# Optimization experiments

Hardware: AMD Instinct MI355X
Metric: run time of the kernel (lower is better)

## Reference

```python
import jax, jax.numpy as jnp
import numpy as np

N, D, O, E = 100000, 32, 64, 1600000

def setup_inputs() -> dict:
    key = jax.random.key(0)
    ks = jax.random.split(key, 6)
    x = jax.random.normal(ks[0], (N, D), dtype=jnp.float32)
    edge_index = jax.random.randint(ks[1], (2, E), 0, N, dtype=jnp.int64)
    edge_attr = jax.random.uniform(ks[2], (E, 1), dtype=jnp.float32)
    # nodec MLP params (stored as [in, out]; equiv to torch Linear weight.T)
    W1 = jax.random.normal(ks[3], (3 * D, O), dtype=jnp.float32) * (1.0 / np.sqrt(3 * D))
    b1 = jnp.zeros((O,), dtype=jnp.float32)
    W2 = jax.random.normal(ks[4], (O, O), dtype=jnp.float32) * (1.0 / np.sqrt(O))
    b2 = jnp.zeros((O,), dtype=jnp.float32)
    return {"x": x, "edge_index": edge_index, "edge_attr": edge_attr,
            "W1": W1, "b1": b1, "W2": W2, "b2": b2}

def reference(x, edge_index, edge_attr, W1, b1, W2, b2):
    row, col = edge_index[0], edge_index[1]
    n = x.shape[0]
    # gather, weight by edge_attr, scatter-add into destination nodes
    mi = jax.ops.segment_sum(edge_attr * x[row], col, num_segments=n)  # [N, D]
    mo = jax.ops.segment_sum(edge_attr * x[col], row, num_segments=n)  # [N, D]
    M = jnp.concatenate([mi, mo, x], axis=-1)  # [N, 3D]
    h = jnp.tanh(M @ W1 + b1)
    return jnp.tanh(h @ W2 + b2)
```

## Files before the change

### kernel.cpp

```cpp
#include <hip/hip_runtime.h>
#include <hip/hip_bf16.h>


#define DFEAT 32
#define OFEAT 64
#define EPB   2048
#define KEYS_PER_BIN 128
#define MAXBIN 2048
#define CAP   3072

typedef unsigned long long u64;

__device__ __forceinline__ float rdlane(float v, int l) {
    return __int_as_float(__builtin_amdgcn_readlane(__float_as_int(v), l));
}

__global__ __launch_bounds__(256) void hist_part(
    const int* __restrict__ ei, int* __restrict__ blockhist, int E, int NBIN)
{
    __shared__ int lh[MAXBIN];
    int blk = blockIdx.x;
    for (int i = threadIdx.x; i < NBIN; i += 256) lh[i] = 0;
    __syncthreads();
    int e0 = blk * EPB;
    #pragma unroll
    for (int j = 0; j < 8; ++j) {
        int e = e0 + j * 256 + threadIdx.x;
        if (e < E) {
            int r = ei[e], c = ei[E + e];
            atomicAdd(&lh[(2 * c) >> 7], 1);
            atomicAdd(&lh[(2 * r + 1) >> 7], 1);
        }
    }
    __syncthreads();
    for (int i = threadIdx.x; i < NBIN; i += 256)
        blockhist[(long long)blk * NBIN + i] = lh[i];
}

__global__ __launch_bounds__(64) void colscan(
    const int* __restrict__ blockhist, int* __restrict__ ofsT,
    int* __restrict__ bintotal, int nPB, int NBIN)
{
    int bin  = blockIdx.x;
    int lane = threadIdx.x;
    int run = 0;
    for (int b0 = 0; b0 < nPB; b0 += 64) {
        int b = b0 + lane;
        int v = (b < nPB) ? blockhist[(long long)b * NBIN + bin] : 0;
        int s = v;
        #pragma unroll
        for (int d = 1; d < 64; d <<= 1) {
            int t = __shfl_up(s, d, 64);
            if (lane >= d) s += t;
        }
        if (b < nPB) ofsT[(long long)bin * nPB + b] = s - v + run;
        run += __shfl(s, 63, 64);
    }
    if (lane == 0) bintotal[bin] = run;
}

__global__ __launch_bounds__(1024) void scan_bins(
    const int* __restrict__ bintotal, int* __restrict__ binbase, int NBIN)
{
    __shared__ int s[1024];
    int t = threadIdx.x;
    int i0 = 2 * t, i1 = 2 * t + 1;
    int p0 = (i0 < NBIN) ? ((bintotal[i0] + 1) & ~1) : 0;
    int p1 = (i1 < NBIN) ? ((bintotal[i1] + 1) & ~1) : 0;
    int v = p0 + p1;
    s[t] = v;
    __syncthreads();
    for (int o = 1; o < 1024; o <<= 1) {
        int u = (t >= o) ? s[t - o] : 0;
        __syncthreads();
        s[t] += u;
        __syncthreads();
    }
    int excl = s[t] - v;
    if (i0 < NBIN) binbase[i0] = excl;
    if (i1 < NBIN) binbase[i1] = excl + p0;
}

__global__ __launch_bounds__(256) void partition_kernel(
    const int* __restrict__ ei, const float* __restrict__ ea,
    const int* __restrict__ ofsT, const int* __restrict__ binbase,
    u64* __restrict__ pay, int E, int NBIN, int nPB)
{
    __shared__ int lofs[MAXBIN + 1];
    __shared__ int lcur[MAXBIN];
    __shared__ int lbase[MAXBIN];
    __shared__ u64 stag[2 * EPB];
    __shared__ unsigned short binof[2 * EPB];
    int blk = blockIdx.x, tid = threadIdx.x;
    int e0 = blk * EPB;

    for (int i = tid; i < NBIN; i += 256) lcur[i] = 0;
    __syncthreads();

    int r[8], c[8]; float a[8]; bool valid[8];
    #pragma unroll
    for (int j = 0; j < 8; ++j) {
        int e = e0 + j * 256 + tid;
        valid[j] = (e < E);
        if (valid[j]) {
            r[j] = ei[e]; c[j] = ei[E + e]; a[j] = ea[e];
            atomicAdd(&lcur[(2 * c[j]) >> 7], 1);
            atomicAdd(&lcur[(2 * r[j] + 1) >> 7], 1);
        }
    }
    __syncthreads();

    if (tid < 64) {
        int runc = 0;
        for (int b0 = 0; b0 < NBIN; b0 += 64) {
            int i = b0 + tid;
            int v = (i < NBIN) ? lcur[i] : 0;
            int s = v;
            #pragma unroll
            for (int d = 1; d < 64; d <<= 1) {
                int t2 = __shfl_up(s, d, 64);
                if (tid >= d) s += t2;
            }
            if (i < NBIN) lofs[i] = s - v + runc;
            runc += __shfl(s, 63, 64);
        }
        if (tid == 0) lofs[NBIN] = runc;
    }
    __syncthreads();

    for (int i = tid; i < NBIN; i += 256) {
        lcur[i] = 0;
        lbase[i] = binbase[i] + ofsT[(long long)i * nPB + blk];
    }
    __syncthreads();

    #pragma unroll
    for (int j = 0; j < 8; ++j) {
        if (valid[j]) {
            unsigned int ab = (unsigned int)__float_as_int(a[j]);
            {
                int key = 2 * c[j]; int bin = key >> 7;
                int t2 = atomicAdd(&lcur[bin], 1);
                int pos = lofs[bin] + t2;
                stag[pos] = ((u64)ab << 32) |
                    (unsigned int)(r[j] | ((key & 127) << 17));
                binof[pos] = (unsigned short)bin;
            }
            {
                int key = 2 * r[j] + 1; int bin = key >> 7;
                int t2 = atomicAdd(&lcur[bin], 1);
                int pos = lofs[bin] + t2;
                stag[pos] = ((u64)ab << 32) |
                    (unsigned int)(c[j] | ((key & 127) << 17));
                binof[pos] = (unsigned short)bin;
            }
        }
    }
    __syncthreads();

    int total = lofs[NBIN];
    for (int i = tid; i < total; i += 256) {
        int bn = binof[i];
        pay[lbase[bn] + (i - lofs[bn])] = stag[i];
    }
}

__global__ __launch_bounds__(512) void accum_sortgather(
    const float* __restrict__ x,
    const int* __restrict__ binbase, const int* __restrict__ bintotal,
    const u64* __restrict__ pay,
    float* __restrict__ mi, float* __restrict__ mo, int NK)
{
    __shared__ u64 srec[CAP];
    __shared__ int lcnt[KEYS_PER_BIN];
    __shared__ int lofs[KEYS_PER_BIN];
    __shared__ int lcur[KEYS_PER_BIN];

    int b = blockIdx.x, tid = threadIdx.x;
    int base = binbase[b];
    int n    = bintotal[b];
    int wid  = tid >> 6;
    int lane = tid & 63;
    int half = lane >> 5;
    int feat = lane & 31;

    float accA[4], accB[4], accC[4], accD[4];
    #pragma unroll
    for (int p = 0; p < 4; ++p) {
        accA[p] = 0.0f; accB[p] = 0.0f; accC[p] = 0.0f; accD[p] = 0.0f;
    }

    for (int c0 = 0; c0 < n; c0 += CAP) {
        int cn = min(n - c0, CAP);
        if (tid < KEYS_PER_BIN) lcnt[tid] = 0;
        __syncthreads();
        for (int i = tid; i < cn; i += 512)
            atomicAdd(&lcnt[((int)pay[base + c0 + i] >> 17) & 127], 1);
        __syncthreads();
        if (tid < 64) {
            int v0 = lcnt[2 * tid], v1 = lcnt[2 * tid + 1];
            int s = v0 + v1, ss = s;
            #pragma unroll
            for (int d = 1; d < 64; d <<= 1) {
                int t = __shfl_up(ss, d, 64);
                if (tid >= d) ss += t;
            }
            int excl = ss - s;
            lofs[2 * tid] = excl;      lofs[2 * tid + 1] = excl + v0;
            lcur[2 * tid] = excl;      lcur[2 * tid + 1] = excl + v0;
        }
        __syncthreads();
        for (int i = tid; i < cn; i += 512) {
            u64 v = pay[base + c0 + i];
            int t2 = atomicAdd(&lcur[((int)v >> 17) & 127], 1);
            srec[t2] = v;
        }
        __syncthreads();

        #pragma unroll
        for (int p = 0; p < 4; ++p) {
            int kb = wid * 16 + 4 * p;
            int s0 = lofs[kb + 0], e0 = s0 + lcnt[kb + 0];
            int s1 = lofs[kb + 1], e1 = s1 + lcnt[kb + 1];
            int s2 = lofs[kb + 2], e2 = s2 + lcnt[kb + 2];
            int s3 = lofs[kb + 3], e3 = s3 + lcnt[kb + 3];
            int i0 = s0 + half, i1 = s1 + half, i2 = s2 + half, i3 = s3 + half;
            float a0 = accA[p], a1 = accB[p], a2 = accC[p], a3 = accD[p];
            while (i0 < e0 && i1 < e1 && i2 < e2 && i3 < e3) {
                u64 r0 = srec[i0], r1 = srec[i1], r2 = srec[i2], r3 = srec[i3];
                float x0 = x[(long long)((int)r0 & 0x1FFFF) * DFEAT + feat];
                float x1 = x[(long long)((int)r1 & 0x1FFFF) * DFEAT + feat];
                float x2 = x[(long long)((int)r2 & 0x1FFFF) * DFEAT + feat];
                float x3 = x[(long long)((int)r3 & 0x1FFFF) * DFEAT + feat];
                a0 = fmaf(__int_as_float((int)(r0 >> 32)), x0, a0);
                a1 = fmaf(__int_as_float((int)(r1 >> 32)), x1, a1);
                a2 = fmaf(__int_as_float((int)(r2 >> 32)), x2, a2);
                a3 = fmaf(__int_as_float((int)(r3 >> 32)), x3, a3);
                i0 += 2; i1 += 2; i2 += 2; i3 += 2;
            }
            while (i0 < e0) {
                u64 rr = srec[i0];
                a0 = fmaf(__int_as_float((int)(rr >> 32)),
                          x[(long long)((int)rr & 0x1FFFF) * DFEAT + feat], a0);
                i0 += 2;
            }
            while (i1 < e1) {
                u64 rr = srec[i1];
                a1 = fmaf(__int_as_float((int)(rr >> 32)),
                          x[(long long)((int)rr & 0x1FFFF) * DFEAT + feat], a1);
                i1 += 2;
            }
            while (i2 < e2) {
                u64 rr = srec[i2];
                a2 = fmaf(__int_as_float((int)(rr >> 32)),
                          x[(long long)((int)rr & 0x1FFFF) * DFEAT + feat], a2);
                i2 += 2;
            }
            while (i3 < e3) {
                u64 rr = srec[i3];
                a3 = fmaf(__int_as_float((int)(rr >> 32)),
                          x[(long long)((int)rr & 0x1FFFF) * DFEAT + feat], a3);
                i3 += 2;
            }
            accA[p] = a0; accB[p] = a1; accC[p] = a2; accD[p] = a3;
        }
        __syncthreads();
    }

    int key0 = b * KEYS_PER_BIN + wid * 16;
    #pragma unroll
    for (int p = 0; p < 4; ++p) {
        float t0 = accA[p] + __shfl_xor(accA[p], 32, 64);
        float t1 = accB[p] + __shfl_xor(accB[p], 32, 64);
        float t2 = accC[p] + __shfl_xor(accC[p], 32, 64);
        float t3 = accD[p] + __shfl_xor(accD[p], 32, 64);
        float vA = half ? t2 : t0;
        float vB = half ? t3 : t1;
        int gkA = key0 + 4 * p + (half ? 2 : 0);
        int gkB = gkA + 1;
        if (gkA < NK) {
            int node = gkA >> 1;
            ((gkA & 1) ? mo : mi)[(long long)node * DFEAT + feat] = vA;
        }
        if (gkB < NK) {
            int node = gkB >> 1;
            ((gkB & 1) ? mo : mi)[(long long)node * DFEAT + feat] = vB;
        }
    }
}

__global__ __launch_bounds__(256) void edge_scatter_kernel(
    const float* __restrict__ x, const int* __restrict__ ei,
    const float* __restrict__ ea,
    float* __restrict__ mi, float* __restrict__ mo, int E)
{
    long long tid = (long long)blockIdx.x * blockDim.x + threadIdx.x;
    long long total = (long long)E * 8;
    if (tid >= total) return;
    int e = (int)(tid >> 3);
    int q = (int)(tid & 7);
    int r = ei[e];
    int c = ei[E + e];
    float a = ea[e];
    const float4* x4 = (const float4*)x;
    float4 xr = x4[(long long)r * 8 + q];
    float4 xc = x4[(long long)c * 8 + q];
    float* mip = mi + (long long)c * DFEAT + q * 4;
    float* mop = mo + (long long)r * DFEAT + q * 4;
    atomicAdd(mip + 0, a * xr.x); atomicAdd(mip + 1, a * xr.y);
    atomicAdd(mip + 2, a * xr.z); atomicAdd(mip + 3, a * xr.w);
    atomicAdd(mop + 0, a * xc.x); atomicAdd(mop + 1, a * xc.y);
    atomicAdd(mop + 2, a * xc.z); atomicAdd(mop + 3, a * xc.w);
}

__global__ __launch_bounds__(256) void mlp_reg_kernel(
    const float* __restrict__ mi, const float* __restrict__ mo,
    const float* __restrict__ x,
    const float* __restrict__ W1, const float* __restrict__ b1,
    const float* __restrict__ W2, const float* __restrict__ b2,
    float* __restrict__ out, int N)
{
    int o   = threadIdx.x & 63;
    int wid = threadIdx.x >> 6;

    float w1r[96], w2r[64];
    #pragma unroll
    for (int k = 0; k < 96; ++k) w1r[k] = W1[k * 64 + o];
    #pragma unroll
    for (int k = 0; k < 64; ++k) w2r[k] = W2[k * 64 + o];
    float bias1 = b1[o];
    float bias2 = b2[o];

    int stride = gridDim.x * 4;
    for (int node = blockIdx.x * 4 + wid; node < N; node += stride) {
        long long nb = (long long)node * DFEAT;
        float m01 = (o < 32) ? mi[nb + o] : mo[nb + (o - 32)];
        float m2v = (o < 32) ? x[nb + o] : 0.0f;

        float a0 = bias1, a1 = 0.0f, a2 = 0.0f, a3 = 0.0f;
        #pragma unroll
        for (int k = 0; k < 64; k += 4) {
            a0 = fmaf(rdlane(m01, k + 0), w1r[k + 0], a0);
            a1 = fmaf(rdlane(m01, k + 1), w1r[k + 1], a1);
            a2 = fmaf(rdlane(m01, k + 2), w1r[k + 2], a2);
            a3 = fmaf(rdlane(m01, k + 3), w1r[k + 3], a3);
        }
        #pragma unroll
        for (int k = 0; k < 32; k += 4) {
            a0 = fmaf(rdlane(m2v, k + 0), w1r[64 + k + 0], a0);
            a1 = fmaf(rdlane(m2v, k + 1), w1r[64 + k + 1], a1);
            a2 = fmaf(rdlane(m2v, k + 2), w1r[64 + k + 2], a2);
            a3 = fmaf(rdlane(m2v, k + 3), w1r[64 + k + 3], a3);
        }
        float h = tanhf(((a0 + a1) + (a2 + a3)));

        float c0 = bias2, c1 = 0.0f, c2 = 0.0f, c3 = 0.0f;
        #pragma unroll
        for (int k = 0; k < 64; k += 4) {
            c0 = fmaf(rdlane(h, k + 0), w2r[k + 0], c0);
            c1 = fmaf(rdlane(h, k + 1), w2r[k + 1], c1);
            c2 = fmaf(rdlane(h, k + 2), w2r[k + 2], c2);
            c3 = fmaf(rdlane(h, k + 3), w2r[k + 3], c3);
        }
        out[(long long)node * OFEAT + o] = tanhf(((c0 + c1) + (c2 + c3)));
    }
}

extern "C" void kernel_launch(void* const* d_in, const int* in_sizes, int n_in,
                              void* d_out, int out_size, void* d_ws, size_t ws_size,
                              hipStream_t stream) {
    const float* x  = (const float*)d_in[0];
    const int*   ei = (const int*)  d_in[1];
    const float* ea = (const float*)d_in[2];
    const float* W1 = (const float*)d_in[3];
    const float* b1 = (const float*)d_in[4];
    const float* W2 = (const float*)d_in[5];
    const float* b2 = (const float*)d_in[6];
    float* out = (float*)d_out;

    int N    = in_sizes[0] / DFEAT;
    int E    = in_sizes[2];
    int NK   = 2 * N;
    int NBIN = (NK + KEYS_PER_BIN - 1) / KEYS_PER_BIN;
    int nPB  = (E + EPB - 1) / EPB;

    float* mi = (float*)d_ws;
    float* mo = mi + (size_t)N * DFEAT;

    size_t paySlots = (size_t)2 * E + NBIN;
    size_t need = (size_t)N * DFEAT * 2 * 4
                + paySlots * 8
                + (size_t)nPB * NBIN * 4 * 2
                + (size_t)NBIN * 4 * 2 + 64;

    if (ws_size >= need && N <= (1 << 17) && NBIN <= MAXBIN) {
        u64* pay       = (u64*)(mo + (size_t)N * DFEAT);
        int* blockhist = (int*)(pay + paySlots);
        int* ofsT      = blockhist + (size_t)nPB * NBIN;
        int* bintotal  = ofsT + (size_t)nPB * NBIN;
        int* binbase   = bintotal + NBIN;

        hist_part<<<nPB, 256, 0, stream>>>(ei, blockhist, E, NBIN);
        colscan<<<NBIN, 64, 0, stream>>>(blockhist, ofsT, bintotal, nPB, NBIN);
        scan_bins<<<1, 1024, 0, stream>>>(bintotal, binbase, NBIN);
        partition_kernel<<<nPB, 256, 0, stream>>>(ei, ea, ofsT, binbase,
                                                  pay, E, NBIN, nPB);
        accum_sortgather<<<NBIN, 512, 0, stream>>>(x, binbase, bintotal, pay,
                                                   mi, mo, NK);
    } else {
        hipMemsetAsync(d_ws, 0, (size_t)N * DFEAT * 2 * sizeof(float), stream);
        long long total = (long long)E * 8;
        int nblocks = (int)((total + 255) / 256);
        edge_scatter_kernel<<<nblocks, 256, 0, stream>>>(x, ei, ea, mi, mo, E);
    }

    mlp_reg_kernel<<<512, 256, 0, stream>>>(mi, mo, x, W1, b1, W2, b2, out, N);
}
```

Baseline: 236.1 us.

## Vectorize edge loads, shrink partition LDS, and grid-stride bin accumulation

The histogram and partition kernels now run 512 threads per block, each loading four consecutive edges with int4/float4 vector loads. Partition drops the per-record bin-id array and stores offsets as 16-bit values, finding each record's bin by binary search over the offsets. This cuts LDS use, which may raise occupancy, at the cost of extra search work in the scatter loop. The accumulation kernel launches half as many blocks and loops over bins grid-stride, so two bins run back to back per block.

New measurement: 262.9 us. 11.4% more time.

```diff
diff --git a/kernel.cpp b/kernel.cpp
--- a/kernel.cpp
+++ b/kernel.cpp
@@ -6,7 +6,7 @@
 #define OFEAT 64
 #define EPB   2048
 #define KEYS_PER_BIN 128
-#define MAXBIN 2048
+#define NBINMAX 1568
 #define CAP   3072
 
 typedef unsigned long long u64;
@@ -15,25 +15,33 @@
     return __int_as_float(__builtin_amdgcn_readlane(__float_as_int(v), l));
 }
 
-__global__ __launch_bounds__(256) void hist_part(
+__global__ __launch_bounds__(512) void hist_part(
     const int* __restrict__ ei, int* __restrict__ blockhist, int E, int NBIN)
 {
-    __shared__ int lh[MAXBIN];
-    int blk = blockIdx.x;
-    for (int i = threadIdx.x; i < NBIN; i += 256) lh[i] = 0;
+    __shared__ int lh[NBINMAX];
+    int blk = blockIdx.x, tid = threadIdx.x;
+    for (int i = tid; i < NBIN; i += 512) lh[i] = 0;
     __syncthreads();
     int e0 = blk * EPB;
-    #pragma unroll
-    for (int j = 0; j < 8; ++j) {
-        int e = e0 + j * 256 + threadIdx.x;
-        if (e < E) {
-            int r = ei[e], c = ei[E + e];
-            atomicAdd(&lh[(2 * c) >> 7], 1);
-            atomicAdd(&lh[(2 * r + 1) >> 7], 1);
-        }
-    }
-    __syncthreads();
-    for (int i = threadIdx.x; i < NBIN; i += 256)
+    if (e0 + EPB <= E) {
+        int4 rr = *(const int4*)(ei + e0 + tid * 4);
+        int4 cc = *(const int4*)(ei + E + e0 + tid * 4);
+        atomicAdd(&lh[(2 * cc.x) >> 7], 1); atomicAdd(&lh[(2 * rr.x + 1) >> 7], 1);
+        atomicAdd(&lh[(2 * cc.y) >> 7], 1); atomicAdd(&lh[(2 * rr.y + 1) >> 7], 1);
+        atomicAdd(&lh[(2 * cc.z) >> 7], 1); atomicAdd(&lh[(2 * rr.z + 1) >> 7], 1);
+        atomicAdd(&lh[(2 * cc.w) >> 7], 1); atomicAdd(&lh[(2 * rr.w + 1) >> 7], 1);
+    } else {
+        #pragma unroll
+        for (int j = 0; j < 4; ++j) {
+            int e = e0 + tid * 4 + j;
+            if (e < E) {
+                atomicAdd(&lh[(2 * ei[E + e]) >> 7], 1);
+                atomicAdd(&lh[(2 * ei[e] + 1) >> 7], 1);
+            }
+        }
+    }
+    __syncthreads();
+    for (int i = tid; i < NBIN; i += 512)
         blockhist[(long long)blk * NBIN + i] = lh[i];
 }
 
@@ -81,32 +89,44 @@
     if (i1 < NBIN) binbase[i1] = excl + p0;
 }
 
-__global__ __launch_bounds__(256) void partition_kernel(
+__global__ __launch_bounds__(512) void partition_kernel(
     const int* __restrict__ ei, const float* __restrict__ ea,
     const int* __restrict__ ofsT, const int* __restrict__ binbase,
     u64* __restrict__ pay, int E, int NBIN, int nPB)
 {
-    __shared__ int lofs[MAXBIN + 1];
-    __shared__ int lcur[MAXBIN];
-    __shared__ int lbase[MAXBIN];
+    __shared__ unsigned short lofsw[NBINMAX + 1];
+    __shared__ int lcur[NBINMAX];
+    __shared__ int lbase[NBINMAX];
     __shared__ u64 stag[2 * EPB];
-    __shared__ unsigned short binof[2 * EPB];
     int blk = blockIdx.x, tid = threadIdx.x;
     int e0 = blk * EPB;
 
-    for (int i = tid; i < NBIN; i += 256) lcur[i] = 0;
-    __syncthreads();
-
-    int r[8], c[8]; float a[8]; bool valid[8];
-    #pragma unroll
-    for (int j = 0; j < 8; ++j) {
-        int e = e0 + j * 256 + tid;
-        valid[j] = (e < E);
-        if (valid[j]) {
-            r[j] = ei[e]; c[j] = ei[E + e]; a[j] = ea[e];
-            atomicAdd(&lcur[(2 * c[j]) >> 7], 1);
-            atomicAdd(&lcur[(2 * r[j] + 1) >> 7], 1);
-        }
+    for (int i = tid; i < NBIN; i += 512) lcur[i] = 0;
+    __syncthreads();
+
+    int4 rr, cc; float4 av; bool full = (e0 + EPB <= E);
+    if (full) {
+        rr = *(const int4*)(ei + e0 + tid * 4);
+        cc = *(const int4*)(ei + E + e0 + tid * 4);
+        av = *(const float4*)(ea + e0 + tid * 4);
+        atomicAdd(&lcur[(2 * cc.x) >> 7], 1); atomicAdd(&lcur[(2 * rr.x + 1) >> 7], 1);
+        atomicAdd(&lcur[(2 * cc.y) >> 7], 1); atomicAdd(&lcur[(2 * rr.y + 1) >> 7], 1);
+        atomicAdd(&lcur[(2 * cc.z) >> 7], 1); atomicAdd(&lcur[(2 * rr.z + 1) >> 7], 1);
+        atomicAdd(&lcur[(2 * cc.w) >> 7], 1); atomicAdd(&lcur[(2 * rr.w + 1) >> 7], 1);
+    } else {
+        int rs[4], cs[4]; float as[4];
+        #pragma unroll
+        for (int j = 0; j < 4; ++j) {
+            int e = e0 + tid * 4 + j;
+            if (e < E) {
+                rs[j] = ei[e]; cs[j] = ei[E + e]; as[j] = ea[e];
+                atomicAdd(&lcur[(2 * cs[j]) >> 7], 1);
+                atomicAdd(&lcur[(2 * rs[j] + 1) >> 7], 1);
+            } else { rs[j] = 0; cs[j] = 0; as[j] = 0.0f; }
+        }
+        rr = make_int4(rs[0], rs[1], rs[2], rs[3]);
+        cc = make_int4(cs[0], cs[1], cs[2], cs[3]);
+        av = make_float4(as[0], as[1], as[2], as[3]);
     }
     __syncthreads();
 
@@ -121,47 +141,53 @@
                 int t2 = __shfl_up(s, d, 64);
                 if (tid >= d) s += t2;
             }
-            if (i < NBIN) lofs[i] = s - v + runc;
+            if (i < NBIN) lofsw[i] = (unsigned short)(s - v + runc);
             runc += __shfl(s, 63, 64);
         }
-        if (tid == 0) lofs[NBIN] = runc;
-    }
-    __syncthreads();
-
-    for (int i = tid; i < NBIN; i += 256) {
+        if (tid == 0) lofsw[NBIN] = (unsigned short)runc;
+    }
+    __syncthreads();
+
+    for (int i = tid; i < NBIN; i += 512) {
         lcur[i] = 0;
         lbase[i] = binbase[i] + ofsT[(long long)i * nPB + blk];
     }
     __syncthreads();
 
-    #pragma unroll
-    for (int j = 0; j < 8; ++j) {
-        if (valid[j]) {
-            unsigned int ab = (unsigned int)__float_as_int(a[j]);
-            {
-                int key = 2 * c[j]; int bin = key >> 7;
-                int t2 = atomicAdd(&lcur[bin], 1);
-                int pos = lofs[bin] + t2;
-                stag[pos] = ((u64)ab << 32) |
-                    (unsigned int)(r[j] | ((key & 127) << 17));
-                binof[pos] = (unsigned short)bin;
-            }
-            {
-                int key = 2 * r[j] + 1; int bin = key >> 7;
-                int t2 = atomicAdd(&lcur[bin], 1);
-                int pos = lofs[bin] + t2;
-                stag[pos] = ((u64)ab << 32) |
-                    (unsigned int)(c[j] | ((key & 127) << 17));
-                binof[pos] = (unsigned short)bin;
-            }
-        }
-    }
-    __syncthreads();
-
-    int total = lofs[NBIN];
-    for (int i = tid; i < total; i += 256) {
-        int bn = binof[i];
-        pay[lbase[bn] + (i - lofs[bn])] = stag[i];
+    {
+        int rs[4] = {rr.x, rr.y, rr.z, rr.w};
+        int cs[4] = {cc.x, cc.y, cc.z, cc.w};
+        float as[4] = {av.x, av.y, av.z, av.w};
+        #pragma unroll
+        for (int j = 0; j < 4; ++j) {
+            int e = e0 + tid * 4 + j;
+            if (e < E) {
+                unsigned int ab = (unsigned int)__float_as_int(as[j]);
+                {
+                    int key = 2 * cs[j]; int bin = key >> 7;
+                    int t2 = atomicAdd(&lcur[bin], 1);
+                    stag[(int)lofsw[bin] + t2] = ((u64)ab << 32) |
+                        (unsigned int)(rs[j] | ((key & 127) << 17));
+                }
+                {
+                    int key = 2 * rs[j] + 1; int bin = key >> 7;
+                    int t2 = atomicAdd(&lcur[bin], 1);
+                    stag[(int)lofsw[bin] + t2] = ((u64)ab << 32) |
+                        (unsigned int)(cs[j] | ((key & 127) << 17));
+                }
+            }
+        }
+    }
+    __syncthreads();
+
+    int total = lofsw[NBIN];
+    for (int i = tid; i < total; i += 512) {
+        int lo = 0, hi = NBIN;
+        while (hi - lo > 1) {
+            int mid = (lo + hi) >> 1;
+            if ((int)lofsw[mid] <= i) lo = mid; else hi = mid;
+        }
+        pay[lbase[lo] + (i - (int)lofsw[lo])] = stag[i];
     }
 }
 
@@ -169,123 +195,127 @@
     const float* __restrict__ x,
     const int* __restrict__ binbase, const int* __restrict__ bintotal,
     const u64* __restrict__ pay,
-    float* __restrict__ mi, float* __restrict__ mo, int NK)
+    float* __restrict__ mi, float* __restrict__ mo, int NK, int NBIN)
 {
     __shared__ u64 srec[CAP];
     __shared__ int lcnt[KEYS_PER_BIN];
     __shared__ int lofs[KEYS_PER_BIN];
     __shared__ int lcur[KEYS_PER_BIN];
 
-    int b = blockIdx.x, tid = threadIdx.x;
-    int base = binbase[b];
-    int n    = bintotal[b];
+    int tid = threadIdx.x;
     int wid  = tid >> 6;
     int lane = tid & 63;
     int half = lane >> 5;
     int feat = lane & 31;
 
-    float accA[4], accB[4], accC[4], accD[4];
-    #pragma unroll
-    for (int p = 0; p < 4; ++p) {
-        accA[p] = 0.0f; accB[p] = 0.0f; accC[p] = 0.0f; accD[p] = 0.0f;
-    }
-
-    for (int c0 = 0; c0 < n; c0 += CAP) {
-        int cn = min(n - c0, CAP);
-        if (tid < KEYS_PER_BIN) lcnt[tid] = 0;
+    for (int b = blockIdx.x; b < NBIN; b += gridDim.x) {
+        int base = binbase[b];
+        int n    = bintotal[b];
+
+        float accA[4], accB[4], accC[4], accD[4];
+        #pragma unroll
+        for (int p = 0; p < 4; ++p) {
+            accA[p] = 0.0f; accB[p] = 0.0f; accC[p] = 0.0f; accD[p] = 0.0f;
+        }
+
+        for (int c0 = 0; c0 < n; c0 += CAP) {
+            int cn = min(n - c0, CAP);
+            if (tid < KEYS_PER_BIN) lcnt[tid] = 0;
+            __syncthreads();
+            for (int i = tid; i < cn; i += 512)
+                atomicAdd(&lcnt[((int)pay[base + c0 + i] >> 17) & 127], 1);
+            __syncthreads();
+            if (tid < 64) {
+                int v0 = lcnt[2 * tid], v1 = lcnt[2 * tid + 1];
+                int s = v0 + v1, ss = s;
+                #pragma unroll
+                for (int d = 1; d < 64; d <<= 1) {
+                    int t = __shfl_up(ss, d, 64);
+                    if (tid >= d) ss += t;
+                }
+                int excl = ss - s;
+                lofs[2 * tid] = excl;      lofs[2 * tid + 1] = excl + v0;
+                lcur[2 * tid] = excl;      lcur[2 * tid + 1] = excl + v0;
+            }
+            __syncthreads();
+            for (int i = tid; i < cn; i += 512) {
+                u64 v = pay[base + c0 + i];
+                int t2 = atomicAdd(&lcur[((int)v >> 17) & 127], 1);
+                srec[t2] = v;
+            }
+            __syncthreads();
+
+            #pragma unroll
+            for (int p = 0; p < 4; ++p) {
+                int kb = wid * 16 + 4 * p;
+                int s0 = lofs[kb + 0], e0 = s0 + lcnt[kb + 0];
+                int s1 = lofs[kb + 1], e1 = s1 + lcnt[kb + 1];
+                int s2 = lofs[kb + 2], e2 = s2 + lcnt[kb + 2];
+                int s3 = lofs[kb + 3], e3 = s3 + lcnt[kb + 3];
+                int i0 = s0 + half, i1 = s1 + half, i2 = s2 + half, i3 = s3 + half;
+                float a0 = accA[p], a1 = accB[p], a2 = accC[p], a3 = accD[p];
+                while (i0 < e0 && i1 < e1 && i2 < e2 && i3 < e3) {
+                    u64 r0 = srec[i0], r1 = srec[i1], r2 = srec[i2], r3 = srec[i3];
+                    float x0 = x[(long long)((int)r0 & 0x1FFFF) * DFEAT + feat];
+                    float x1 = x[(long long)((int)r1 & 0x1FFFF) * DFEAT + feat];
+                    float x2 = x[(long long)((int)r2 & 0x1FFFF) * DFEAT + feat];
+                    float x3 = x[(long long)((int)r3 & 0x1FFFF) * DFEAT + feat];
+                    a0 = fmaf(__int_as_float((int)(r0 >> 32)), x0, a0);
+                    a1 = fmaf(__int_as_float((int)(r1 >> 32)), x1, a1);
+                    a2 = fmaf(__int_as_float((int)(r2 >> 32)), x2, a2);
+                    a3 = fmaf(__int_as_float((int)(r3 >> 32)), x3, a3);
+                    i0 += 2; i1 += 2; i2 += 2; i3 += 2;
+                }
+                while (i0 < e0) {
+                    u64 rr = srec[i0];
+                    a0 = fmaf(__int_as_float((int)(rr >> 32)),
+                              x[(long long)((int)rr & 0x1FFFF) * DFEAT + feat], a0);
+                    i0 += 2;
+                }
+                while (i1 < e1) {
+                    u64 rr = srec[i1];
+                    a1 = fmaf(__int_as_float((int)(rr >> 32)),
+                              x[(long long)((int)rr & 0x1FFFF) * DFEAT + feat], a1);
+                    i1 += 2;
+                }
+                while (i2 < e2) {
+                    u64 rr = srec[i2];
+                    a2 = fmaf(__int_as_float((int)(rr >> 32)),
+                              x[(long long)((int)rr & 0x1FFFF) * DFEAT + feat], a2);
+                    i2 += 2;
+                }
+                while (i3 < e3) {
+                    u64 rr = srec[i3];
+                    a3 = fmaf(__int_as_float((int)(rr >> 32)),
+                              x[(long long)((int)rr & 0x1FFFF) * DFEAT + feat], a3);
+                    i3 += 2;
+                }
+                accA[p] = a0; accB[p] = a1; accC[p] = a2; accD[p] = a3;
+            }
+            __syncthreads();
+        }
+
+        int key0 = b * KEYS_PER_BIN + wid * 16;
+        #pragma unroll
+        for (int p = 0; p < 4; ++p) {
+            float t0 = accA[p] + __shfl_xor(accA[p], 32, 64);
+            float t1 = accB[p] + __shfl_xor(accB[p], 32, 64);
+            float t2 = accC[p] + __shfl_xor(accC[p], 32, 64);
+            float t3 = accD[p] + __shfl_xor(accD[p], 32, 64);
+            float vA = half ? t2 : t0;
+            float vB = half ? t3 : t1;
+            int gkA = key0 + 4 * p + (half ? 2 : 0);
+            int gkB = gkA + 1;
+            if (gkA < NK) {
+                int node = gkA >> 1;
+                ((gkA & 1) ? mo : mi)[(long long)node * DFEAT + feat] = vA;
+            }
+            if (gkB < NK) {
+                int node = gkB >> 1;
+                ((gkB & 1) ? mo : mi)[(long long)node * DFEAT + feat] = vB;
+            }
+        }
         __syncthreads();
-        for (int i = tid; i < cn; i += 512)
-            atomicAdd(&lcnt[((int)pay[base + c0 + i] >> 17) & 127], 1);
-        __syncthreads();
-        if (tid < 64) {
-            int v0 = lcnt[2 * tid], v1 = lcnt[2 * tid + 1];
-            int s = v0 + v1, ss = s;
-            #pragma unroll
-            for (int d = 1; d < 64; d <<= 1) {
-                int t = __shfl_up(ss, d, 64);
-                if (tid >= d) ss += t;
-            }
-            int excl = ss - s;
-            lofs[2 * tid] = excl;      lofs[2 * tid + 1] = excl + v0;
-            lcur[2 * tid] = excl;      lcur[2 * tid + 1] = excl + v0;
-        }
-        __syncthreads();
-        for (int i = tid; i < cn; i += 512) {
-            u64 v = pay[base + c0 + i];
-            int t2 = atomicAdd(&lcur[((int)v >> 17) & 127], 1);
-            srec[t2] = v;
-        }
-        __syncthreads();
-
-        #pragma unroll
-        for (int p = 0; p < 4; ++p) {
-            int kb = wid * 16 + 4 * p;
-            int s0 = lofs[kb + 0], e0 = s0 + lcnt[kb + 0];
-            int s1 = lofs[kb + 1], e1 = s1 + lcnt[kb + 1];
-            int s2 = lofs[kb + 2], e2 = s2 + lcnt[kb + 2];
-            int s3 = lofs[kb + 3], e3 = s3 + lcnt[kb + 3];
-            int i0 = s0 + half, i1 = s1 + half, i2 = s2 + half, i3 = s3 + half;
-            float a0 = accA[p], a1 = accB[p], a2 = accC[p], a3 = accD[p];
-            while (i0 < e0 && i1 < e1 && i2 < e2 && i3 < e3) {
-                u64 r0 = srec[i0], r1 = srec[i1], r2 = srec[i2], r3 = srec[i3];
-                float x0 = x[(long long)((int)r0 & 0x1FFFF) * DFEAT + feat];
-                float x1 = x[(long long)((int)r1 & 0x1FFFF) * DFEAT + feat];
-                float x2 = x[(long long)((int)r2 & 0x1FFFF) * DFEAT + feat];
-                float x3 = x[(long long)((int)r3 & 0x1FFFF) * DFEAT + feat];
-                a0 = fmaf(__int_as_float((int)(r0 >> 32)), x0, a0);
-                a1 = fmaf(__int_as_float((int)(r1 >> 32)), x1, a1);
-                a2 = fmaf(__int_as_float((int)(r2 >> 32)), x2, a2);
-                a3 = fmaf(__int_as_float((int)(r3 >> 32)), x3, a3);
-                i0 += 2; i1 += 2; i2 += 2; i3 += 2;
-            }
-            while (i0 < e0) {
-                u64 rr = srec[i0];
-                a0 = fmaf(__int_as_float((int)(rr >> 32)),
-                          x[(long long)((int)rr & 0x1FFFF) * DFEAT + feat], a0);
-                i0 += 2;
-            }
-            while (i1 < e1) {
-                u64 rr = srec[i1];
-                a1 = fmaf(__int_as_float((int)(rr >> 32)),
-                          x[(long long)((int)rr & 0x1FFFF) * DFEAT + feat], a1);
-                i1 += 2;
-            }
-            while (i2 < e2) {
-                u64 rr = srec[i2];
-                a2 = fmaf(__int_as_float((int)(rr >> 32)),
-                          x[(long long)((int)rr & 0x1FFFF) * DFEAT + feat], a2);
-                i2 += 2;
-            }
-            while (i3 < e3) {
-                u64 rr = srec[i3];
-                a3 = fmaf(__int_as_float((int)(rr >> 32)),
-                          x[(long long)((int)rr & 0x1FFFF) * DFEAT + feat], a3);
-                i3 += 2;
-            }
-            accA[p] = a0; accB[p] = a1; accC[p] = a2; accD[p] = a3;
-        }
-        __syncthreads();
-    }
-
-    int key0 = b * KEYS_PER_BIN + wid * 16;
-    #pragma unroll
-    for (int p = 0; p < 4; ++p) {
-        float t0 = accA[p] + __shfl_xor(accA[p], 32, 64);
-        float t1 = accB[p] + __shfl_xor(accB[p], 32, 64);
-        float t2 = accC[p] + __shfl_xor(accC[p], 32, 64);
-        float t3 = accD[p] + __shfl_xor(accD[p], 32, 64);
-        float vA = half ? t2 : t0;
-        float vB = half ? t3 : t1;
-        int gkA = key0 + 4 * p + (half ? 2 : 0);
-        int gkB = gkA + 1;
-        if (gkA < NK) {
-            int node = gkA >> 1;
-            ((gkA & 1) ? mo : mi)[(long long)node * DFEAT + feat] = vA;
-        }
-        if (gkB < NK) {
-            int node = gkB >> 1;
-            ((gkB & 1) ? mo : mi)[(long long)node * DFEAT + feat] = vB;
-        }
     }
 }
 
@@ -393,20 +423,21 @@
                 + (size_t)nPB * NBIN * 4 * 2
                 + (size_t)NBIN * 4 * 2 + 64;
 
-    if (ws_size >= need && N <= (1 << 17) && NBIN <= MAXBIN) {
+    if (ws_size >= need && N <= (1 << 17) && NBIN <= NBINMAX) {
         u64* pay       = (u64*)(mo + (size_t)N * DFEAT);
         int* blockhist = (int*)(pay + paySlots);
         int* ofsT      = blockhist + (size_t)nPB * NBIN;
         int* bintotal  = ofsT + (size_t)nPB * NBIN;
         int* binbase   = bintotal + NBIN;
 
-        hist_part<<<nPB, 256, 0, stream>>>(ei, blockhist, E, NBIN);
+        hist_part<<<nPB, 512, 0, stream>>>(ei, blockhist, E, NBIN);
         colscan<<<NBIN, 64, 0, stream>>>(blockhist, ofsT, bintotal, nPB, NBIN);
         scan_bins<<<1, 1024, 0, stream>>>(bintotal, binbase, NBIN);
-        partition_kernel<<<nPB, 256, 0, stream>>>(ei, ea, ofsT, binbase,
+        partition_kernel<<<nPB, 512, 0, stream>>>(ei, ea, ofsT, binbase,
                                                   pay, E, NBIN, nPB);
-        accum_sortgather<<<NBIN, 512, 0, stream>>>(x, binbase, bintotal, pay,
-                                                   mi, mo, NK);
+        int agrid = (NBIN + 1) / 2;
+        accum_sortgather<<<agrid, 512, 0, stream>>>(x, binbase, bintotal, pay,
+                                                    mi, mo, NK, NBIN);
     } else {
         hipMemsetAsync(d_ws, 0, (size_t)N * DFEAT * 2 * sizeof(float), stream);
         long long total = (long long)E * 8;
```
